# Kernel tuning notes

Hardware: AMD Instinct MI355X
Metric: run time of the kernel (lower is better)

The kernel has to match this reference:

```python
import jax, jax.numpy as jnp
from jax import lax
import numpy as np

INPUT_DIM = 64
EMB_DIM = 24   # hardcoded Dense(24) in MyLSTM
UNITS = 128    # hardcoded LSTM_cell(128)


def setup_inputs() -> dict:
    key = jax.random.key(0)
    ks = jax.random.split(key, 12)
    B, T, D = 1024, 2048, INPUT_DIM
    gin = EMB_DIM + UNITS  # 152: concat([x_emb, h])
    s_emb = 1.0 / np.sqrt(D)
    s_g = 1.0 / np.sqrt(gin)
    s_o = 1.0 / np.sqrt(UNITS)
    return {
        "x": jax.random.normal(ks[0], (B, T, D), jnp.float32),
        "W_emb": jax.random.normal(ks[1], (D, EMB_DIM), jnp.float32) * s_emb,
        "b_emb": jnp.zeros((EMB_DIM,), jnp.float32),
        "Wf": jax.random.normal(ks[2], (gin, UNITS), jnp.float32) * s_g,
        "bf": jnp.ones((UNITS,), jnp.float32),  # forget bias init = ones
        "Wi": jax.random.normal(ks[3], (gin, UNITS), jnp.float32) * s_g,
        "bi": jnp.zeros((UNITS,), jnp.float32),
        "Wg": jax.random.normal(ks[4], (gin, UNITS), jnp.float32) * s_g,
        "bg": jnp.zeros((UNITS,), jnp.float32),
        "Wo": jax.random.normal(ks[5], (gin, UNITS), jnp.float32) * s_g,
        "bo": jnp.zeros((UNITS,), jnp.float32),
        "W_out": jax.random.normal(ks[6], (UNITS, 1), jnp.float32) * s_o,
        "b_out": jnp.zeros((1,), jnp.float32),
    }


def reference(x, W_emb, b_emb, Wf, bf, Wi, bi, Wg, bg, Wo, bo, W_out, b_out):
    # embedding: Dense(24, sigmoid) applied per timestep
    e = jax.nn.sigmoid(jnp.einsum("btd,de->bte", x, W_emb) + b_emb)  # [B,T,24]
    B = x.shape[0]
    h0 = jnp.zeros((B, UNITS), x.dtype)
    c0 = jnp.zeros((B, UNITS), x.dtype)

    def step(carry, xt):
        h, c = carry
        z = jnp.concatenate([xt, h], axis=-1)  # [B, 152]
        f = jax.nn.sigmoid(z @ Wf + bf)
        i = jax.nn.sigmoid(z @ Wi + bi)
        g = jnp.tanh(z @ Wg + bg)
        o = jax.nn.sigmoid(z @ Wo + bo)
        c_new = c * f + i * g
        h_new = jnp.tanh(c_new) * o
        return (h_new, c_new), None

    (h_last, _), _ = lax.scan(step, (h0, c0), jnp.swapaxes(e, 0, 1))  # scan over T
    return jax.nn.sigmoid(h_last @ W_out + b_out)  # [B, 1]
```

## Files before the change

kernel.cpp:

```cpp
#include <hip/hip_runtime.h>
#include <hip/hip_bf16.h>

#define T_STEPS 2048
#define BATCH   1024
#define NUNITS  128
#define ROWS    8
#define LOG2E   1.4426950408889634f

typedef __attribute__((ext_vector_type(8))) __bf16 bf16x8;
typedef __attribute__((ext_vector_type(4))) float  f32x4;
typedef __attribute__((ext_vector_type(2))) int    i32x2;

__device__ __forceinline__ float sigm_pre(float xs) {
    return __builtin_amdgcn_rcpf(1.0f + __builtin_amdgcn_exp2f(-xs));
}
__device__ __forceinline__ float tanh_pre(float xs) {
    return fmaf(-2.0f, __builtin_amdgcn_rcpf(1.0f + __builtin_amdgcn_exp2f(xs)), 1.0f);
}
__device__ __forceinline__ float swap_lo(float a, float b) {
    i32x2 r = __builtin_amdgcn_permlane32_swap(__builtin_bit_cast(int, a),
                                               __builtin_bit_cast(int, b),
                                               false, false);
    return __builtin_bit_cast(float, r[0]);
}

__global__ __launch_bounds__(256) void emb_kernel(const float* __restrict__ x,
                                                  const float* __restrict__ Wemb,
                                                  const float* __restrict__ bemb,
                                                  ushort* __restrict__ e_out) {
    int g = blockIdx.x * 256 + threadIdx.x;
    int t = g >> 10;
    int b = g & 1023;
    const float* xr = x + ((size_t)b * T_STEPS + t) * 64;

    float4 xv[16];
#pragma unroll
    for (int i = 0; i < 16; i++) xv[i] = ((const float4*)xr)[i];

    float acc[24];
#pragma unroll
    for (int j = 0; j < 24; j++) acc[j] = bemb[j];

#pragma unroll
    for (int d = 0; d < 64; d++) {
        float xs = ((const float*)xv)[d];
#pragma unroll
        for (int j = 0; j < 24; j++) acc[j] = fmaf(xs, Wemb[d * 24 + j], acc[j]);
    }

    uint outp[12];
#pragma unroll
    for (int p = 0; p < 12; p++) {
        float lo = __builtin_amdgcn_rcpf(1.0f + __builtin_amdgcn_exp2f(-LOG2E * acc[2 * p]));
        float hi = __builtin_amdgcn_rcpf(1.0f + __builtin_amdgcn_exp2f(-LOG2E * acc[2 * p + 1]));
        ushort ulo = __builtin_bit_cast(ushort, (__bf16)lo);
        ushort uhi = __builtin_bit_cast(ushort, (__bf16)hi);
        outp[p] = (uint)ulo | ((uint)uhi << 16);
    }
    uint4* dst = (uint4*)(e_out + (size_t)g * 24);
#pragma unroll
    for (int q = 0; q < 3; q++) dst[q] = ((const uint4*)outp)[q];
}

__global__ __launch_bounds__(512, 1) void lstm_kernel(
    const ushort* __restrict__ e_ws,
    const float* __restrict__ Wf, const float* __restrict__ bf_,
    const float* __restrict__ Wi, const float* __restrict__ bi_,
    const float* __restrict__ Wg, const float* __restrict__ bg_,
    const float* __restrict__ Wo, const float* __restrict__ bo_,
    const float* __restrict__ Wout, const float* __restrict__ bout,
    float* __restrict__ out) {
    __shared__ __align__(16) __bf16 zfrag[2][4][4][16][8];

    const int tid  = threadIdx.x;
    const int lane = tid & 63;
    const int wv   = tid >> 6;
    const int l15  = lane & 15;
    const int kg   = lane >> 4;
    const int r0   = blockIdx.x * ROWS;

    const float* Wp[4] = {Wf, Wi, Wg, Wo};
    const float gsc[4] = {LOG2E, LOG2E, 2.0f * LOG2E, LOG2E};
    const int ucol = wv * 16 + l15;
    bf16x8 wreg[4][5];
#pragma unroll
    for (int gt = 0; gt < 4; gt++) {
#pragma unroll
        for (int ks = 0; ks < 5; ks++) {
#pragma unroll
            for (int j = 0; j < 8; j++) {
                int k = ks * 32 + kg * 8 + j;
                float v = 0.0f;
                if (k < 128) v = Wp[gt][(24 + k) * NUNITS + ucol];
                else if (k < 152) v = Wp[gt][(k - 128) * NUNITS + ucol];
                wreg[gt][ks][j] = (__bf16)(v * gsc[gt]);
            }
        }
    }
    const float* Bp[4] = {bf_, bi_, bg_, bo_};
    f32x4 bias[4];
#pragma unroll
    for (int gt = 0; gt < 4; gt++) {
        float bv = Bp[gt][ucol] * gsc[gt];
#pragma unroll
        for (int r = 0; r < 4; r++) bias[gt][r] = bv;
    }

    for (int i = tid; i < 2 * 4 * 4 * 16 * 8; i += 512) ((__bf16*)zfrag)[i] = (__bf16)0.0f;

    const __bf16* zrd = &zfrag[0][0][kg][l15][0];
    const int q2 = lane >> 4;
    const int row_c0 = ((q2 & 1) << 2) | ((q2 >> 1) << 1);
    __bf16* zwr = &zfrag[0][ucol >> 5][(ucol >> 3) & 3][row_c0][ucol & 7];

    const ushort* elbase = e_ws + ((size_t)(r0 + (l15 & 7)) * 24 + kg * 8);
    const bool eload = (kg < 3) && (l15 < 8);
    bf16x8 e0, e1;
#pragma unroll
    for (int j = 0; j < 8; j++) { e0[j] = (__bf16)0.0f; e1[j] = (__bf16)0.0f; }
    if (eload) {
        e0 = *(const bf16x8*)(const void*)(elbase);
        e1 = *(const bf16x8*)(const void*)(elbase + 24576);
    }

    __syncthreads();

    float c0 = 0.0f, c1 = 0.0f;
    f32x4 eA[4], eB[4];
#pragma unroll
    for (int gt = 0; gt < 4; gt++)
        eA[gt] = __builtin_amdgcn_mfma_f32_16x16x32_bf16(e0, wreg[gt][4], bias[gt], 0, 0, 0);
    if (eload) e0 = *(const bf16x8*)(const void*)(elbase + 2 * 24576);

    auto STEP = [&](int t, int P, f32x4 (&cur)[4], f32x4 (&nxt)[4], bf16x8& enext) {
        const __bf16* zb = zrd + P * 2048;
        bf16x8 z0 = *(const bf16x8*)(const void*)(zb);
        bf16x8 z1 = *(const bf16x8*)(const void*)(zb + 512);
        bf16x8 z2 = *(const bf16x8*)(const void*)(zb + 1024);
        bf16x8 z3 = *(const bf16x8*)(const void*)(zb + 1536);

        f32x4 acc[4];
#pragma unroll
        for (int gt = 0; gt < 4; gt++) {
            acc[gt] = __builtin_amdgcn_mfma_f32_16x16x32_bf16(z0, wreg[gt][0], cur[gt], 0, 0, 0);
            acc[gt] = __builtin_amdgcn_mfma_f32_16x16x32_bf16(z1, wreg[gt][1], acc[gt], 0, 0, 0);
            acc[gt] = __builtin_amdgcn_mfma_f32_16x16x32_bf16(z2, wreg[gt][2], acc[gt], 0, 0, 0);
            acc[gt] = __builtin_amdgcn_mfma_f32_16x16x32_bf16(z3, wreg[gt][3], acc[gt], 0, 0, 0);
        }

#pragma unroll
        for (int gt = 0; gt < 4; gt++)
            nxt[gt] = __builtin_amdgcn_mfma_f32_16x16x32_bf16(enext, wreg[gt][4], bias[gt], 0, 0, 0);
        {
            int tf = t + 3; if (tf > T_STEPS - 1) tf = T_STEPS - 1;
            if (eload) enext = *(const bf16x8*)(const void*)(elbase + (size_t)tf * 24576);
        }

        float g0[4], g1[4];
#pragma unroll
        for (int gt = 0; gt < 4; gt++) {
            g0[gt] = swap_lo(acc[gt][0], acc[gt][2]);
            g1[gt] = swap_lo(acc[gt][1], acc[gt][3]);
        }

        float fg0 = sigm_pre(g0[0]), fg1 = sigm_pre(g1[0]);
        float ig0 = sigm_pre(g0[1]), ig1 = sigm_pre(g1[1]);
        float gg0 = tanh_pre(g0[2]), gg1 = tanh_pre(g1[2]);
        float og0 = sigm_pre(g0[3]), og1 = sigm_pre(g1[3]);
        c0 = fmaf(c0, fg0, ig0 * gg0);
        c1 = fmaf(c1, fg1, ig1 * gg1);
        float h0 = tanh_pre(2.0f * LOG2E * c0) * og0;
        float h1 = tanh_pre(2.0f * LOG2E * c1) * og1;

        __bf16* zw = zwr + (P ^ 1) * 2048;
        zw[0] = (__bf16)h0;
        zw[8] = (__bf16)h1;

        asm volatile("s_waitcnt lgkmcnt(0)" ::: "memory");
        __builtin_amdgcn_s_barrier();
        __builtin_amdgcn_sched_barrier(0);
    };

    for (int t = 0; t < T_STEPS; t += 2) {
        STEP(t,     0, eA, eB, e1);
        STEP(t + 1, 1, eB, eA, e0);
    }

    if (tid < ROWS) {
        float s = bout[0];
#pragma unroll
        for (int k = 0; k < NUNITS; k++)
            s += (float)zfrag[0][k >> 5][(k >> 3) & 3][tid][k & 7] * Wout[k];
        out[r0 + tid] = __builtin_amdgcn_rcpf(1.0f + __builtin_amdgcn_exp2f(-LOG2E * s));
    }
}

extern "C" void kernel_launch(void* const* d_in, const int* in_sizes, int n_in,
                              void* d_out, int out_size, void* d_ws, size_t ws_size,
                              hipStream_t stream) {
    const float* x     = (const float*)d_in[0];
    const float* Wemb  = (const float*)d_in[1];
    const float* bemb  = (const float*)d_in[2];
    const float* Wf    = (const float*)d_in[3];
    const float* bf_   = (const float*)d_in[4];
    const float* Wi    = (const float*)d_in[5];
    const float* bi_   = (const float*)d_in[6];
    const float* Wg    = (const float*)d_in[7];
    const float* bg_   = (const float*)d_in[8];
    const float* Wo    = (const float*)d_in[9];
    const float* bo_   = (const float*)d_in[10];
    const float* Wout  = (const float*)d_in[11];
    const float* bout  = (const float*)d_in[12];
    float* out = (float*)d_out;
    ushort* e_ws = (ushort*)d_ws;

    int nrows = BATCH * T_STEPS;
    emb_kernel<<<nrows / 256, 256, 0, stream>>>(x, Wemb, bemb, e_ws);
    lstm_kernel<<<BATCH / ROWS, 512, 0, stream>>>(e_ws, Wf, bf_, Wi, bi_, Wg, bg_,
                                                  Wo, bo_, Wout, bout, out);
}
```

Baseline: 1.447 ms.

## Split LSTM rows into two interleaved groups to overlap MFMA with gate math

Splits each block's 8 batch rows into two independent groups of 4 and alternates half-steps between them. The h-fragment reads for one group are issued while the other group's gates are computed, hiding LDS latency and the recurrent dependency chain. The MFMA reduction is also split into two independent accumulator chains, and launch bounds allow two blocks per CU. Each step now needs twice as many barriers, and MFMA tiles run half-empty because only 4 of 16 rows are active.

```diff
diff --git a/kernel.cpp b/kernel.cpp
--- a/kernel.cpp
+++ b/kernel.cpp
@@ -62,7 +62,7 @@
     for (int q = 0; q < 3; q++) dst[q] = ((const uint4*)outp)[q];
 }
 
-__global__ __launch_bounds__(512, 1) void lstm_kernel(
+__global__ __launch_bounds__(512, 2) void lstm_kernel(
     const ushort* __restrict__ e_ws,
     const float* __restrict__ Wf, const float* __restrict__ bf_,
     const float* __restrict__ Wi, const float* __restrict__ bi_,
@@ -70,7 +70,7 @@
     const float* __restrict__ Wo, const float* __restrict__ bo_,
     const float* __restrict__ Wout, const float* __restrict__ bout,
     float* __restrict__ out) {
-    __shared__ __align__(16) __bf16 zfrag[2][4][4][16][8];
+    __shared__ __align__(16) __bf16 zbuf[2][4][4][6][8];
 
     const int tid  = threadIdx.x;
     const int lane = tid & 63;
@@ -105,92 +105,118 @@
 #pragma unroll
         for (int r = 0; r < 4; r++) bias[gt][r] = bv;
     }
-
-    for (int i = tid; i < 2 * 4 * 4 * 16 * 8; i += 512) ((__bf16*)zfrag)[i] = (__bf16)0.0f;
-
-    const __bf16* zrd = &zfrag[0][0][kg][l15][0];
-    const int q2 = lane >> 4;
-    const int row_c0 = ((q2 & 1) << 2) | ((q2 >> 1) << 1);
-    __bf16* zwr = &zfrag[0][ucol >> 5][(ucol >> 3) & 3][row_c0][ucol & 7];
-
-    const ushort* elbase = e_ws + ((size_t)(r0 + (l15 & 7)) * 24 + kg * 8);
-    const bool eload = (kg < 3) && (l15 < 8);
-    bf16x8 e0, e1;
-#pragma unroll
-    for (int j = 0; j < 8; j++) { e0[j] = (__bf16)0.0f; e1[j] = (__bf16)0.0f; }
+    const f32x4 zero4 = {0.0f, 0.0f, 0.0f, 0.0f};
+
+    for (int i = tid; i < 2 * 4 * 4 * 6 * 8; i += 512) ((__bf16*)zbuf)[i] = (__bf16)0.0f;
+
+    __bf16* zbase = &zbuf[0][0][0][0][0];
+    const bool rd_act = (l15 < 4);
+    const __bf16* rdA = zbase + kg * 48 + l15 * 8;
+    const __bf16* rdB = rdA + 768;
+    const int w_m0 = (lane >= 32) ? 2 : 0;
+    const bool wact = (((lane >> 4) & 1) == 0);
+    __bf16* wA = zbase + (ucol >> 5) * 192 + ((ucol >> 3) & 3) * 48 + w_m0 * 8 + (ucol & 7);
+    __bf16* wB = wA + 768;
+
+    const bool eload = (kg < 3) && rd_act;
+    const ushort* elbA = e_ws + ((size_t)(r0 + (l15 & 3)) * 24 + kg * 8);
+    const ushort* elbB = elbA + 4 * 24;
+    bf16x8 eA0, eA1, eB0, eB1;
+#pragma unroll
+    for (int j = 0; j < 8; j++) { eA0[j] = (__bf16)0; eA1[j] = (__bf16)0; eB0[j] = (__bf16)0; eB1[j] = (__bf16)0; }
     if (eload) {
-        e0 = *(const bf16x8*)(const void*)(elbase);
-        e1 = *(const bf16x8*)(const void*)(elbase + 24576);
+        eA0 = *(const bf16x8*)(const void*)(elbA);
+        eA1 = *(const bf16x8*)(const void*)(elbA + 24576);
+        eB0 = *(const bf16x8*)(const void*)(elbB);
+        eB1 = *(const bf16x8*)(const void*)(elbB + 24576);
     }
 
     __syncthreads();
 
-    float c0 = 0.0f, c1 = 0.0f;
-    f32x4 eA[4], eB[4];
-#pragma unroll
-    for (int gt = 0; gt < 4; gt++)
-        eA[gt] = __builtin_amdgcn_mfma_f32_16x16x32_bf16(e0, wreg[gt][4], bias[gt], 0, 0, 0);
-    if (eload) e0 = *(const bf16x8*)(const void*)(elbase + 2 * 24576);
-
-    auto STEP = [&](int t, int P, f32x4 (&cur)[4], f32x4 (&nxt)[4], bf16x8& enext) {
-        const __bf16* zb = zrd + P * 2048;
-        bf16x8 z0 = *(const bf16x8*)(const void*)(zb);
-        bf16x8 z1 = *(const bf16x8*)(const void*)(zb + 512);
-        bf16x8 z2 = *(const bf16x8*)(const void*)(zb + 1024);
-        bf16x8 z3 = *(const bf16x8*)(const void*)(zb + 1536);
-
-        f32x4 acc[4];
+    f32x4 eaccA[4], eaccB[4];
+#pragma unroll
+    for (int gt = 0; gt < 4; gt++) {
+        eaccA[gt] = __builtin_amdgcn_mfma_f32_16x16x32_bf16(eA0, wreg[gt][4], bias[gt], 0, 0, 0);
+        eaccB[gt] = __builtin_amdgcn_mfma_f32_16x16x32_bf16(eB0, wreg[gt][4], bias[gt], 0, 0, 0);
+    }
+    if (eload) {
+        eA0 = *(const bf16x8*)(const void*)(elbA + 2 * 24576);
+        eB0 = *(const bf16x8*)(const void*)(elbB + 2 * 24576);
+    }
+
+    bf16x8 zrA[4], zrB[4];
+#pragma unroll
+    for (int q = 0; q < 4; q++)
+#pragma unroll
+        for (int j = 0; j < 8; j++) { zrA[q][j] = (__bf16)0; zrB[q][j] = (__bf16)0; }
+
+    float cA0 = 0, cA1 = 0, cB0 = 0, cB1 = 0;
+
+    auto HALF = [&](int t, __bf16* zw, const __bf16* zo_rd,
+                    bf16x8 (&zr)[4], bf16x8 (&ozr)[4],
+                    f32x4 (&eacc)[4], bf16x8& ering, const ushort* elb,
+                    float& cc0, float& cc1) {
+        if (rd_act) {
+            ozr[0] = *(const bf16x8*)(const void*)(zo_rd);
+            ozr[1] = *(const bf16x8*)(const void*)(zo_rd + 192);
+            ozr[2] = *(const bf16x8*)(const void*)(zo_rd + 384);
+            ozr[3] = *(const bf16x8*)(const void*)(zo_rd + 576);
+        }
+        f32x4 ca[4], cb[4];
 #pragma unroll
         for (int gt = 0; gt < 4; gt++) {
-            acc[gt] = __builtin_amdgcn_mfma_f32_16x16x32_bf16(z0, wreg[gt][0], cur[gt], 0, 0, 0);
-            acc[gt] = __builtin_amdgcn_mfma_f32_16x16x32_bf16(z1, wreg[gt][1], acc[gt], 0, 0, 0);
-            acc[gt] = __builtin_amdgcn_mfma_f32_16x16x32_bf16(z2, wreg[gt][2], acc[gt], 0, 0, 0);
-            acc[gt] = __builtin_amdgcn_mfma_f32_16x16x32_bf16(z3, wreg[gt][3], acc[gt], 0, 0, 0);
-        }
-
+            ca[gt] = __builtin_amdgcn_mfma_f32_16x16x32_bf16(zr[0], wreg[gt][0], eacc[gt], 0, 0, 0);
+            cb[gt] = __builtin_amdgcn_mfma_f32_16x16x32_bf16(zr[1], wreg[gt][1], zero4, 0, 0, 0);
+        }
+#pragma unroll
+        for (int gt = 0; gt < 4; gt++) {
+            ca[gt] = __builtin_amdgcn_mfma_f32_16x16x32_bf16(zr[2], wreg[gt][2], ca[gt], 0, 0, 0);
+            cb[gt] = __builtin_amdgcn_mfma_f32_16x16x32_bf16(zr[3], wreg[gt][3], cb[gt], 0, 0, 0);
+        }
 #pragma unroll
         for (int gt = 0; gt < 4; gt++)
-            nxt[gt] = __builtin_amdgcn_mfma_f32_16x16x32_bf16(enext, wreg[gt][4], bias[gt], 0, 0, 0);
+            eacc[gt] = __builtin_amdgcn_mfma_f32_16x16x32_bf16(ering, wreg[gt][4], bias[gt], 0, 0, 0);
         {
             int tf = t + 3; if (tf > T_STEPS - 1) tf = T_STEPS - 1;
-            if (eload) enext = *(const bf16x8*)(const void*)(elbase + (size_t)tf * 24576);
-        }
-
+            if (eload) ering = *(const bf16x8*)(const void*)(elb + (size_t)tf * 24576);
+        }
         float g0[4], g1[4];
 #pragma unroll
         for (int gt = 0; gt < 4; gt++) {
-            g0[gt] = swap_lo(acc[gt][0], acc[gt][2]);
-            g1[gt] = swap_lo(acc[gt][1], acc[gt][3]);
-        }
-
+            f32x4 gs = ca[gt] + cb[gt];
+            g0[gt] = swap_lo(gs[0], gs[2]);
+            g1[gt] = swap_lo(gs[1], gs[3]);
+        }
         float fg0 = sigm_pre(g0[0]), fg1 = sigm_pre(g1[0]);
         float ig0 = sigm_pre(g0[1]), ig1 = sigm_pre(g1[1]);
         float gg0 = tanh_pre(g0[2]), gg1 = tanh_pre(g1[2]);
         float og0 = sigm_pre(g0[3]), og1 = sigm_pre(g1[3]);
-        c0 = fmaf(c0, fg0, ig0 * gg0);
-        c1 = fmaf(c1, fg1, ig1 * gg1);
-        float h0 = tanh_pre(2.0f * LOG2E * c0) * og0;
-        float h1 = tanh_pre(2.0f * LOG2E * c1) * og1;
-
-        __bf16* zw = zwr + (P ^ 1) * 2048;
-        zw[0] = (__bf16)h0;
-        zw[8] = (__bf16)h1;
-
+        cc0 = fmaf(cc0, fg0, ig0 * gg0);
+        cc1 = fmaf(cc1, fg1, ig1 * gg1);
+        float h0 = tanh_pre(2.0f * LOG2E * cc0) * og0;
+        float h1 = tanh_pre(2.0f * LOG2E * cc1) * og1;
+        if (wact) {
+            zw[0] = (__bf16)h0;
+            zw[8] = (__bf16)h1;
+        }
         asm volatile("s_waitcnt lgkmcnt(0)" ::: "memory");
         __builtin_amdgcn_s_barrier();
         __builtin_amdgcn_sched_barrier(0);
     };
 
     for (int t = 0; t < T_STEPS; t += 2) {
-        STEP(t,     0, eA, eB, e1);
-        STEP(t + 1, 1, eB, eA, e0);
+        HALF(t,     wB, rdA, zrB, zrA, eaccB, eB1, elbB, cB0, cB1);
+        HALF(t,     wA, rdB, zrA, zrB, eaccA, eA1, elbA, cA0, cA1);
+        HALF(t + 1, wB, rdA, zrB, zrA, eaccB, eB0, elbB, cB0, cB1);
+        HALF(t + 1, wA, rdB, zrA, zrB, eaccA, eA0, elbA, cA0, cA1);
     }
 
     if (tid < ROWS) {
+        int g = tid >> 2, lr = tid & 3;
         float s = bout[0];
 #pragma unroll
         for (int k = 0; k < NUNITS; k++)
-            s += (float)zfrag[0][k >> 5][(k >> 3) & 3][tid][k & 7] * Wout[k];
+            s += (float)zbuf[g][k >> 5][(k >> 3) & 3][lr][k & 7] * Wout[k];
         out[r0 + tid] = __builtin_amdgcn_rcpf(1.0f + __builtin_amdgcn_exp2f(-LOG2E * s));
     }
 }
```

Measured after the change: 2.836 ms. 1.96x slower.

## Quantize recurrent weights and hidden state to int8 for i8 MFMA

Applied to the files above, without the earlier changes.

Replaces the bf16 recurrent matmul (16 MFMA 16x16x32 per step) with int8 MFMA 16x16x64 (8 per step), using per-column symmetric weight scales and a fixed 1/127 scale for h. The hidden state is stored in LDS as int8, which halves the shared-memory footprint and read traffic per step. Dequantization is folded into an FMA with the precomputed embedding/bias contribution. This risks accuracy loss over 2048 recurrent steps from 8-bit quantization of h and weights.

```diff
diff --git a/kernel.cpp b/kernel.cpp
--- a/kernel.cpp
+++ b/kernel.cpp
@@ -10,6 +10,7 @@
 typedef __attribute__((ext_vector_type(8))) __bf16 bf16x8;
 typedef __attribute__((ext_vector_type(4))) float  f32x4;
 typedef __attribute__((ext_vector_type(2))) int    i32x2;
+typedef __attribute__((ext_vector_type(4))) int    int4v;
 
 __device__ __forceinline__ float sigm_pre(float xs) {
     return __builtin_amdgcn_rcpf(1.0f + __builtin_amdgcn_exp2f(-xs));
@@ -70,7 +71,7 @@
     const float* __restrict__ Wo, const float* __restrict__ bo_,
     const float* __restrict__ Wout, const float* __restrict__ bout,
     float* __restrict__ out) {
-    __shared__ __align__(16) __bf16 zfrag[2][4][4][16][8];
+    __shared__ __align__(16) char zq[2][2][4][16][16];
 
     const int tid  = threadIdx.x;
     const int lane = tid & 63;
@@ -82,19 +83,39 @@
     const float* Wp[4] = {Wf, Wi, Wg, Wo};
     const float gsc[4] = {LOG2E, LOG2E, 2.0f * LOG2E, LOG2E};
     const int ucol = wv * 16 + l15;
-    bf16x8 wreg[4][5];
+
+    int4v wq[4][2];
+    float fct[4];
 #pragma unroll
     for (int gt = 0; gt < 4; gt++) {
-#pragma unroll
-        for (int ks = 0; ks < 5; ks++) {
-#pragma unroll
-            for (int j = 0; j < 8; j++) {
-                int k = ks * 32 + kg * 8 + j;
-                float v = 0.0f;
-                if (k < 128) v = Wp[gt][(24 + k) * NUNITS + ucol];
-                else if (k < 152) v = Wp[gt][(k - 128) * NUNITS + ucol];
-                wreg[gt][ks][j] = (__bf16)(v * gsc[gt]);
+        float amax = 1e-20f;
+        for (int k = 0; k < 128; k++)
+            amax = fmaxf(amax, fabsf(Wp[gt][(24 + k) * NUNITS + ucol] * gsc[gt]));
+        float isq = 127.0f / amax;
+        fct[gt] = amax / (127.0f * 127.0f);
+#pragma unroll
+        for (int ks = 0; ks < 2; ks++) {
+#pragma unroll
+            for (int w = 0; w < 4; w++) {
+                int word = 0;
+#pragma unroll
+                for (int b = 0; b < 4; b++) {
+                    int k = ks * 64 + kg * 16 + w * 4 + b;
+                    int q = (int)__builtin_rintf(Wp[gt][(24 + k) * NUNITS + ucol] * gsc[gt] * isq);
+                    word |= (q & 255) << (8 * b);
+                }
+                wq[gt][ks][w] = word;
             }
+        }
+    }
+    bf16x8 wrege[4];
+#pragma unroll
+    for (int gt = 0; gt < 4; gt++) {
+#pragma unroll
+        for (int j = 0; j < 8; j++) {
+            int k = 128 + kg * 8 + j;
+            float v = (k < 152) ? Wp[gt][(k - 128) * NUNITS + ucol] : 0.0f;
+            wrege[gt][j] = (__bf16)(v * gsc[gt]);
         }
     }
     const float* Bp[4] = {bf_, bi_, bg_, bo_};
@@ -105,13 +126,14 @@
 #pragma unroll
         for (int r = 0; r < 4; r++) bias[gt][r] = bv;
     }
-
-    for (int i = tid; i < 2 * 4 * 4 * 16 * 8; i += 512) ((__bf16*)zfrag)[i] = (__bf16)0.0f;
-
-    const __bf16* zrd = &zfrag[0][0][kg][l15][0];
+    const int4v zeroi = {0, 0, 0, 0};
+
+    for (int i = tid; i < 2 * 2 * 4 * 16 * 16 / 4; i += 512) ((int*)zq)[i] = 0;
+
+    const char* zrd = &zq[0][0][kg][l15][0];
     const int q2 = lane >> 4;
     const int row_c0 = ((q2 & 1) << 2) | ((q2 >> 1) << 1);
-    __bf16* zwr = &zfrag[0][ucol >> 5][(ucol >> 3) & 3][row_c0][ucol & 7];
+    char* zwr = &zq[0][ucol >> 6][(ucol >> 4) & 3][row_c0][ucol & 15];
 
     const ushort* elbase = e_ws + ((size_t)(r0 + (l15 & 7)) * 24 + kg * 8);
     const bool eload = (kg < 3) && (l15 < 8);
@@ -129,28 +151,25 @@
     f32x4 eA[4], eB[4];
 #pragma unroll
     for (int gt = 0; gt < 4; gt++)
-        eA[gt] = __builtin_amdgcn_mfma_f32_16x16x32_bf16(e0, wreg[gt][4], bias[gt], 0, 0, 0);
+        eA[gt] = __builtin_amdgcn_mfma_f32_16x16x32_bf16(e0, wrege[gt], bias[gt], 0, 0, 0);
     if (eload) e0 = *(const bf16x8*)(const void*)(elbase + 2 * 24576);
 
     auto STEP = [&](int t, int P, f32x4 (&cur)[4], f32x4 (&nxt)[4], bf16x8& enext) {
-        const __bf16* zb = zrd + P * 2048;
-        bf16x8 z0 = *(const bf16x8*)(const void*)(zb);
-        bf16x8 z1 = *(const bf16x8*)(const void*)(zb + 512);
-        bf16x8 z2 = *(const bf16x8*)(const void*)(zb + 1024);
-        bf16x8 z3 = *(const bf16x8*)(const void*)(zb + 1536);
-
-        f32x4 acc[4];
-#pragma unroll
-        for (int gt = 0; gt < 4; gt++) {
-            acc[gt] = __builtin_amdgcn_mfma_f32_16x16x32_bf16(z0, wreg[gt][0], cur[gt], 0, 0, 0);
-            acc[gt] = __builtin_amdgcn_mfma_f32_16x16x32_bf16(z1, wreg[gt][1], acc[gt], 0, 0, 0);
-            acc[gt] = __builtin_amdgcn_mfma_f32_16x16x32_bf16(z2, wreg[gt][2], acc[gt], 0, 0, 0);
-            acc[gt] = __builtin_amdgcn_mfma_f32_16x16x32_bf16(z3, wreg[gt][3], acc[gt], 0, 0, 0);
-        }
-
+        const char* zb = zrd + P * 2048;
+        int4v z0 = *(const int4v*)(const void*)(zb);
+        int4v z1 = *(const int4v*)(const void*)(zb + 1024);
+
+        int4v acc[4];
 #pragma unroll
         for (int gt = 0; gt < 4; gt++)
-            nxt[gt] = __builtin_amdgcn_mfma_f32_16x16x32_bf16(enext, wreg[gt][4], bias[gt], 0, 0, 0);
+            acc[gt] = __builtin_amdgcn_mfma_i32_16x16x64_i8(z0, wq[gt][0], zeroi, 0, 0, 0);
+#pragma unroll
+        for (int gt = 0; gt < 4; gt++)
+            acc[gt] = __builtin_amdgcn_mfma_i32_16x16x64_i8(z1, wq[gt][1], acc[gt], 0, 0, 0);
+
+#pragma unroll
+        for (int gt = 0; gt < 4; gt++)
+            nxt[gt] = __builtin_amdgcn_mfma_f32_16x16x32_bf16(enext, wrege[gt], bias[gt], 0, 0, 0);
         {
             int tf = t + 3; if (tf > T_STEPS - 1) tf = T_STEPS - 1;
             if (eload) enext = *(const bf16x8*)(const void*)(elbase + (size_t)tf * 24576);
@@ -159,8 +178,12 @@
         float g0[4], g1[4];
 #pragma unroll
         for (int gt = 0; gt < 4; gt++) {
-            g0[gt] = swap_lo(acc[gt][0], acc[gt][2]);
-            g1[gt] = swap_lo(acc[gt][1], acc[gt][3]);
+            float p0 = fmaf((float)acc[gt][0], fct[gt], cur[gt][0]);
+            float p1 = fmaf((float)acc[gt][1], fct[gt], cur[gt][1]);
+            float p2 = fmaf((float)acc[gt][2], fct[gt], cur[gt][2]);
+            float p3 = fmaf((float)acc[gt][3], fct[gt], cur[gt][3]);
+            g0[gt] = swap_lo(p0, p2);
+            g1[gt] = swap_lo(p1, p3);
         }
 
         float fg0 = sigm_pre(g0[0]), fg1 = sigm_pre(g1[0]);
@@ -172,9 +195,11 @@
         float h0 = tanh_pre(2.0f * LOG2E * c0) * og0;
         float h1 = tanh_pre(2.0f * LOG2E * c1) * og1;
 
-        __bf16* zw = zwr + (P ^ 1) * 2048;
-        zw[0] = (__bf16)h0;
-        zw[8] = (__bf16)h1;
+        int q0i = (int)__builtin_rintf(h0 * 127.0f);
+        int q1i = (int)__builtin_rintf(h1 * 127.0f);
+        char* zw = zwr + (P ^ 1) * 2048;
+        zw[0]  = (char)q0i;
+        zw[16] = (char)q1i;
 
         asm volatile("s_waitcnt lgkmcnt(0)" ::: "memory");
         __builtin_amdgcn_s_barrier();
@@ -187,10 +212,11 @@
     }
 
     if (tid < ROWS) {
-        float s = bout[0];
+        float s2 = 0.0f;
 #pragma unroll
         for (int k = 0; k < NUNITS; k++)
-            s += (float)zfrag[0][k >> 5][(k >> 3) & 3][tid][k & 7] * Wout[k];
+            s2 += (float)zq[0][k >> 6][(k >> 4) & 3][tid][k & 15] * Wout[k];
+        float s = s2 * (1.0f / 127.0f) + bout[0];
         out[r0 + tid] = __builtin_amdgcn_rcpf(1.0f + __builtin_amdgcn_exp2f(-LOG2E * s));
     }
 }
```

Measured after the change: 1.541 ms. 6.5% more time.
